# Kernel optimization log

Hardware: AMD Instinct MI355X
Metric: run time of the kernel (lower is better)

Reference implementation:

```python
import jax, jax.numpy as jnp
import numpy as np

N_NODES = 100000
N_EDGES = 1000000
IN_DIM = 64
OUT_DIM = 64
N_REL = 4


def setup_inputs() -> dict:
    key = jax.random.key(0)
    k1, k2, k3, k4, k5, k6 = jax.random.split(key, 6)
    x = jax.random.normal(k1, (N_NODES, IN_DIM), dtype=jnp.float32)
    edge_index = jax.random.randint(k2, (2, N_EDGES), 0, N_NODES, dtype=jnp.int64)
    edge_type = jax.random.randint(k3, (N_EDGES,), 0, N_REL, dtype=jnp.int64)
    # learned params of FastRGCNConv (no basis/block decomposition)
    scale = 1.0 / np.sqrt(IN_DIM)
    weight = jax.random.normal(k4, (N_REL, IN_DIM, OUT_DIM), dtype=jnp.float32) * scale
    root = jax.random.normal(k5, (IN_DIM, OUT_DIM), dtype=jnp.float32) * scale
    bias = jax.random.normal(k6, (OUT_DIM,), dtype=jnp.float32) * 0.01
    return {"x": x, "edge_index": edge_index, "edge_type": edge_type,
            "weight": weight, "root": root, "bias": bias}


def reference(x, edge_index, edge_type, weight, root, bias):
    # FastRGCNConv (aggr='mean', root_weight=True) + Tanh; dropout in eval mode (identity).
    src, dst = edge_index[0], edge_index[1]
    n = x.shape[0]
    # Transform once per relation, then gather per edge: [R, N, out]
    h = jnp.einsum('ni,rio->rno', x, weight)
    msg = h[edge_type, src]                                   # [E, out]
    agg = jax.ops.segment_sum(msg, dst, num_segments=n)       # [N, out]
    cnt = jax.ops.segment_sum(jnp.ones((msg.shape[0],), x.dtype), dst,
                              num_segments=n)                 # in-degree
    agg = agg / jnp.maximum(cnt, 1.0)[:, None]
    out = agg + x @ root + bias
    return jnp.tanh(out)
```

## Files before the change

### kernel.cpp

```cpp
#include <hip/hip_runtime.h>
#include <hip/hip_fp16.h>
#include <math.h>

#define N_NODES 100000
#define N_EDGES 1000000
#define IN_DIM 64
#define OUT_DIM 64
#define CAP 32
#define NB_BKT 512
#define DPB 196
#define QB 2304
#define BINA_BLOCKS 256
#define BINA_CHUNK 3907

typedef __attribute__((ext_vector_type(8)))  short bf16x8;
typedef __attribute__((ext_vector_type(16))) float f32x16;
typedef __attribute__((ext_vector_type(8)))  unsigned short u16x8;
typedef __attribute__((ext_vector_type(4)))  unsigned short u16x4;

__device__ __forceinline__ unsigned short f2bf(float f) {
    unsigned int u = __float_as_uint(f);
    u = (u + 0x7fffu + ((u >> 16) & 1u)) >> 16;
    return (unsigned short)u;
}
__device__ __forceinline__ float bf2f(unsigned short h) {
    return __uint_as_float(((unsigned int)h) << 16);
}
__device__ __forceinline__ __half2 asH2(unsigned int u) {
    union { unsigned int u; __half2 h; } c; c.u = u; return c.h;
}
__device__ __forceinline__ unsigned int asU32(__half2 h) {
    union { unsigned int u; __half2 h; } c; c.h = h; return c.u;
}

__global__ __launch_bounds__(256) void k_prep(
    const float* __restrict__ x,
    const float* __restrict__ weight, const float* __restrict__ root,
    unsigned short* __restrict__ xb, unsigned short* __restrict__ xh,
    unsigned short* __restrict__ wt_hi, unsigned short* __restrict__ wt_lo,
    int* __restrict__ qcnt)
{
    int u = blockIdx.x * 256 + threadIdx.x;
    if (u < NB_BKT) qcnt[u] = 0;
    if (u < 64 * 320) {
        int n = u / 320, k = u - n * 320;
        float v = (k < 256) ? weight[k * 64 + n] : root[(k - 256) * 64 + n];
        unsigned short h = f2bf(v);
        wt_hi[u] = h;
        wt_lo[u] = f2bf(v - bf2f(h));
    }
    if (u >= N_NODES * 16) return;
    float4 v = *(const float4*)(x + (size_t)u * 4);
    u16x4 hb;
    hb[0] = f2bf(v.x); hb[1] = f2bf(v.y); hb[2] = f2bf(v.z); hb[3] = f2bf(v.w);
    *(u16x4*)(xb + (size_t)u * 4) = hb;
    uint2 st;
    st.x = asU32(__floats2half2_rn(v.x, v.y));
    st.y = asU32(__floats2half2_rn(v.z, v.w));
    *(uint2*)(xh + (size_t)u * 4) = st;
}

__global__ __launch_bounds__(512) void k_binA(const int* __restrict__ ei,
                                              const int* __restrict__ et,
                                              int* __restrict__ qcnt,
                                              unsigned int* __restrict__ queue) {
    __shared__ int hist[NB_BKT], base[NB_BKT], cur[NB_BKT];
    int tid = threadIdx.x;
    for (int b = tid; b < NB_BKT; b += 512) { hist[b] = 0; cur[b] = 0; }
    __syncthreads();
    int b0 = blockIdx.x * BINA_CHUNK;
    int b1 = b0 + BINA_CHUNK; if (b1 > N_EDGES) b1 = N_EDGES;
    for (int e = b0 + tid; e < b1; e += 512)
        atomicAdd(&hist[ei[N_EDGES + e] / DPB], 1);
    __syncthreads();
    for (int b = tid; b < NB_BKT; b += 512)
        base[b] = atomicAdd(&qcnt[b], hist[b]);
    __syncthreads();
    for (int e = b0 + tid; e < b1; e += 512) {
        int d = ei[N_EDGES + e];
        int bkt = d / DPB;
        int ld = d - bkt * DPB;
        int pos = base[bkt] + atomicAdd(&cur[bkt], 1);
        if (pos < QB) {
            queue[(size_t)bkt * QB + pos] =
                ((unsigned)ld << 19) | (unsigned)((ei[e] << 2) | (et[e] & 3));
        }
    }
}

__global__ __launch_bounds__(256) void k_binB(const int* __restrict__ qcnt,
                                              const unsigned int* __restrict__ queue,
                                              int* __restrict__ cnt,
                                              int* __restrict__ slots) {
    __shared__ int lcnt[DPB];
    __shared__ int lslot[DPB * CAP];
    int tid = threadIdx.x;
    int bkt = blockIdx.x;
    int d0 = bkt * DPB;
    for (int i = tid; i < DPB; i += 256) lcnt[i] = 0;
    __syncthreads();
    int n = qcnt[bkt]; if (n > QB) n = QB;
    const unsigned int* q = queue + (size_t)bkt * QB;
    for (int i = tid; i < n; i += 256) {
        unsigned int r = q[i];
        int d = (int)(r >> 19);
        int pos = atomicAdd(&lcnt[d], 1);
        if (pos < CAP) lslot[(d << 5) + pos] = (int)(r & 0x7ffffu);
    }
    __syncthreads();
    for (int i = tid; i < DPB; i += 256) {
        int g = d0 + i;
        if (g < N_NODES) cnt[g] = lcnt[i];
    }
    for (int i = tid; i < DPB * CAP / 4; i += 256) {
        int g0 = d0 * CAP + i * 4;
        if (g0 < N_NODES * CAP) {
            int4 v = *(const int4*)&lslot[i * 4];
            *(int4*)&slots[g0] = v;
        }
    }
}

__global__ __launch_bounds__(256) void k_gather(
    const int* __restrict__ cnt, const int* __restrict__ slots,
    const unsigned short* __restrict__ xh, unsigned short* __restrict__ agg)
{
    int wv = threadIdx.x >> 6, ln = threadIdx.x & 63;
    int node = blockIdx.x * 4 + wv;
    int es = ln >> 4;
    int fq = ln & 15;

    int deg = cnt[node];
    int m = (deg < CAP) ? deg : CAP;
    float inv = 1.0f / fmaxf((float)deg, 1.0f);

    int sv = slots[(node << 5) + (ln & 31)];

    __half2 a0_01 = asH2(0), a0_23 = asH2(0);
    __half2 a1_01 = asH2(0), a1_23 = asH2(0);
    __half2 a2_01 = asH2(0), a2_23 = asH2(0);
    __half2 a3_01 = asH2(0), a3_23 = asH2(0);

    int T = (m + 3) >> 2;
    for (int t = 0; t < T; ++t) {
        int i = es + (t << 2);
        int p = __shfl(sv, i);
        bool valid = (i < m);
        if (!valid) p = 0;
        int r = p & 3;
        uint2 v = *(const uint2*)(xh + ((size_t)(p >> 2) << 6) + (fq << 2));
        __half2 h01 = asH2(v.x), h23 = asH2(v.y);
        __half2 m0 = asH2((valid && r == 0) ? 0x3C003C00u : 0u);
        __half2 m1 = asH2((valid && r == 1) ? 0x3C003C00u : 0u);
        __half2 m2 = asH2((valid && r == 2) ? 0x3C003C00u : 0u);
        __half2 m3 = asH2((valid && r == 3) ? 0x3C003C00u : 0u);
        a0_01 = __hfma2(h01, m0, a0_01); a0_23 = __hfma2(h23, m0, a0_23);
        a1_01 = __hfma2(h01, m1, a1_01); a1_23 = __hfma2(h23, m1, a1_23);
        a2_01 = __hfma2(h01, m2, a2_01); a2_23 = __hfma2(h23, m2, a2_23);
        a3_01 = __hfma2(h01, m3, a3_01); a3_23 = __hfma2(h23, m3, a3_23);
    }

#define REDH(a)                                                        \
    a = __hadd2(a, asH2(__shfl_xor(asU32(a), 16)));                    \
    a = __hadd2(a, asH2(__shfl_xor(asU32(a), 32)));
    REDH(a0_01) REDH(a0_23) REDH(a1_01) REDH(a1_23)
    REDH(a2_01) REDH(a2_23) REDH(a3_01) REDH(a3_23)
#undef REDH

    __half2 w01 = a0_01, w23 = a0_23;
    if (es == 1)      { w01 = a1_01; w23 = a1_23; }
    else if (es == 2) { w01 = a2_01; w23 = a2_23; }
    else if (es == 3) { w01 = a3_01; w23 = a3_23; }
    float2 f01 = __half22float2(w01);
    float2 f23 = __half22float2(w23);
    u16x4 h;
    h[0] = f2bf(f01.x * inv); h[1] = f2bf(f01.y * inv);
    h[2] = f2bf(f23.x * inv); h[3] = f2bf(f23.y * inv);
    *(u16x4*)(agg + (size_t)node * 256 + (ln << 2)) = h;
}

__global__ __launch_bounds__(256) void k_gemm(
    const unsigned short* __restrict__ agg,
    const unsigned short* __restrict__ xb,
    const unsigned short* __restrict__ wt_hi,
    const unsigned short* __restrict__ wt_lo,
    const float* __restrict__ bias, float* __restrict__ out)
{
    __shared__ short As[128 * 64];
    __shared__ short Bh[64 * 64];
    __shared__ short Bl[64 * 64];

    int tid = threadIdx.x;
    int n0 = blockIdx.x * 128;
    int lane = tid & 63, wv = tid >> 6;
    int lr = lane & 31, g = lane >> 5;

    f32x16 acc0 = {}, acc1 = {};

    for (int kc = 0; kc < 5; ++kc) {
        if (kc) __syncthreads();
        #pragma unroll
        for (int i = 0; i < 4; ++i) {
            int u = i * 256 + tid;
            int row = u >> 3, i16 = u & 7;
            int node = n0 + row;
            if (node > N_NODES - 1) node = N_NODES - 1;
            const unsigned short* src = (kc < 4)
                ? (agg + (size_t)node * 256 + kc * 64)
                : (xb + (size_t)node * 64);
            u16x8 v = *(const u16x8*)(src + i16 * 8);
            int off = row * 128 + ((i16 * 16) ^ ((row & 7) << 4));
            *(u16x8*)((char*)As + off) = v;
        }
        #pragma unroll
        for (int i = 0; i < 2; ++i) {
            int u = i * 256 + tid;
            int n = u >> 3, i16 = u & 7;
            size_t s = (size_t)n * 320 + kc * 64 + i16 * 8;
            int off = n * 128 + ((i16 * 16) ^ ((n & 7) << 4));
            *(u16x8*)((char*)Bh + off) = *(const u16x8*)(wt_hi + s);
            *(u16x8*)((char*)Bl + off) = *(const u16x8*)(wt_lo + s);
        }
        __syncthreads();
        int ar = wv * 32 + lr;
        #pragma unroll
        for (int kst = 0; kst < 4; ++kst) {
            int kb = kst * 32 + g * 16;
            int offA = ar * 128 + (kb ^ ((ar & 7) << 4));
            int offB = lr * 128 + (kb ^ ((lr & 7) << 4));
            bf16x8 ah  = *(const bf16x8*)((const char*)As + offA);
            bf16x8 bh0 = *(const bf16x8*)((const char*)Bh + offB);
            bf16x8 bl0 = *(const bf16x8*)((const char*)Bl + offB);
            bf16x8 bh1 = *(const bf16x8*)((const char*)Bh + offB + 32 * 128);
            bf16x8 bl1 = *(const bf16x8*)((const char*)Bl + offB + 32 * 128);
            acc0 = __builtin_amdgcn_mfma_f32_32x32x16_bf16(ah, bh0, acc0, 0, 0, 0);
            acc0 = __builtin_amdgcn_mfma_f32_32x32x16_bf16(ah, bl0, acc0, 0, 0, 0);
            acc1 = __builtin_amdgcn_mfma_f32_32x32x16_bf16(ah, bh1, acc1, 0, 0, 0);
            acc1 = __builtin_amdgcn_mfma_f32_32x32x16_bf16(ah, bl1, acc1, 0, 0, 0);
        }
    }

    float b0 = bias[lr], b1 = bias[32 + lr];
    #pragma unroll
    for (int r = 0; r < 16; ++r) {
        int rowl = (r & 3) + ((r >> 2) << 3) + (g << 2);
        int node = n0 + wv * 32 + rowl;
        if (node < N_NODES) {
            out[(size_t)node * 64 + lr]      = tanhf(acc0[r] + b0);
            out[(size_t)node * 64 + 32 + lr] = tanhf(acc1[r] + b1);
        }
    }
}

extern "C" void kernel_launch(void* const* d_in, const int* in_sizes, int n_in,
                              void* d_out, int out_size, void* d_ws, size_t ws_size,
                              hipStream_t stream) {
    const float* x      = (const float*)d_in[0];
    const int*   ei     = (const int*)d_in[1];
    const int*   et     = (const int*)d_in[2];
    const float* weight = (const float*)d_in[3];
    const float* root   = (const float*)d_in[4];
    const float* bias   = (const float*)d_in[5];
    float* out = (float*)d_out;

    unsigned short* agg   = (unsigned short*)d_ws;
    unsigned short* xb    = agg + (size_t)N_NODES * 256;
    unsigned short* xh    = xb + (size_t)N_NODES * 64;
    unsigned short* wt_hi = xh + (size_t)N_NODES * 64;
    unsigned short* wt_lo = wt_hi + 64 * 320;
    int* cnt   = (int*)(wt_lo + 64 * 320);
    int* slots = cnt + N_NODES;
    int* qcnt  = slots + (size_t)N_NODES * CAP;
    unsigned int* queue = (unsigned int*)(qcnt + NB_BKT);

    k_prep<<<(N_NODES * 16 + 255) / 256, 256, 0, stream>>>(x, weight, root,
                                                           xb, xh, wt_hi, wt_lo,
                                                           qcnt);
    k_binA<<<BINA_BLOCKS, 512, 0, stream>>>(ei, et, qcnt, queue);
    k_binB<<<NB_BKT, 256, 0, stream>>>(qcnt, queue, cnt, slots);
    k_gather<<<N_NODES / 4, 256, 0, stream>>>(cnt, slots, xh, agg);
    k_gemm<<<(N_NODES + 127) / 128, 256, 0, stream>>>(agg, xb, wt_hi, wt_lo,
                                                      bias, out);
}
```

Baseline: 97.12 us.

## Sort edge slots by relation in binning and merge prep with edge binning

Fuses the x/weight conversion kernel with the edge-binning kernel into one launch, branching on block index, and zeroes the queue counters with a memset. The second binning pass now counts edges per (node, relation), prefix-sums the counts, and stores each node's slots grouped by relation with packed per-relation offsets in cnt. The gather kernel can then give each 16-lane group a contiguous run of same-relation edges, so it keeps one accumulator pair instead of four masked ones and skips the cross-group shuffle reduction. In exchange binB reads its queue twice, and packing offsets into 8-bit fields caps the stored total degree at 255, which could break the mean for very high-degree nodes.

```diff
diff --git a/kernel.cpp b/kernel.cpp
--- a/kernel.cpp
+++ b/kernel.cpp
@@ -12,6 +12,7 @@
 #define QB 2304
 #define BINA_BLOCKS 256
 #define BINA_CHUNK 3907
+#define PREP_BLOCKS 3125
 
 typedef __attribute__((ext_vector_type(8)))  short bf16x8;
 typedef __attribute__((ext_vector_type(16))) float f32x16;
@@ -33,57 +34,57 @@
     union { unsigned int u; __half2 h; } c; c.h = h; return c.u;
 }
 
-__global__ __launch_bounds__(256) void k_prep(
+__global__ __launch_bounds__(512) void k_prepA(
     const float* __restrict__ x,
     const float* __restrict__ weight, const float* __restrict__ root,
+    const int* __restrict__ ei, const int* __restrict__ et,
     unsigned short* __restrict__ xb, unsigned short* __restrict__ xh,
     unsigned short* __restrict__ wt_hi, unsigned short* __restrict__ wt_lo,
-    int* __restrict__ qcnt)
+    int* __restrict__ qcnt, unsigned int* __restrict__ queue)
 {
-    int u = blockIdx.x * 256 + threadIdx.x;
-    if (u < NB_BKT) qcnt[u] = 0;
-    if (u < 64 * 320) {
-        int n = u / 320, k = u - n * 320;
-        float v = (k < 256) ? weight[k * 64 + n] : root[(k - 256) * 64 + n];
-        unsigned short h = f2bf(v);
-        wt_hi[u] = h;
-        wt_lo[u] = f2bf(v - bf2f(h));
-    }
-    if (u >= N_NODES * 16) return;
-    float4 v = *(const float4*)(x + (size_t)u * 4);
-    u16x4 hb;
-    hb[0] = f2bf(v.x); hb[1] = f2bf(v.y); hb[2] = f2bf(v.z); hb[3] = f2bf(v.w);
-    *(u16x4*)(xb + (size_t)u * 4) = hb;
-    uint2 st;
-    st.x = asU32(__floats2half2_rn(v.x, v.y));
-    st.y = asU32(__floats2half2_rn(v.z, v.w));
-    *(uint2*)(xh + (size_t)u * 4) = st;
-}
-
-__global__ __launch_bounds__(512) void k_binA(const int* __restrict__ ei,
-                                              const int* __restrict__ et,
-                                              int* __restrict__ qcnt,
-                                              unsigned int* __restrict__ queue) {
     __shared__ int hist[NB_BKT], base[NB_BKT], cur[NB_BKT];
     int tid = threadIdx.x;
-    for (int b = tid; b < NB_BKT; b += 512) { hist[b] = 0; cur[b] = 0; }
-    __syncthreads();
-    int b0 = blockIdx.x * BINA_CHUNK;
-    int b1 = b0 + BINA_CHUNK; if (b1 > N_EDGES) b1 = N_EDGES;
-    for (int e = b0 + tid; e < b1; e += 512)
-        atomicAdd(&hist[ei[N_EDGES + e] / DPB], 1);
-    __syncthreads();
-    for (int b = tid; b < NB_BKT; b += 512)
-        base[b] = atomicAdd(&qcnt[b], hist[b]);
-    __syncthreads();
-    for (int e = b0 + tid; e < b1; e += 512) {
-        int d = ei[N_EDGES + e];
-        int bkt = d / DPB;
-        int ld = d - bkt * DPB;
-        int pos = base[bkt] + atomicAdd(&cur[bkt], 1);
-        if (pos < QB) {
-            queue[(size_t)bkt * QB + pos] =
-                ((unsigned)ld << 19) | (unsigned)((ei[e] << 2) | (et[e] & 3));
+
+    if (blockIdx.x < BINA_BLOCKS) {
+        for (int b = tid; b < NB_BKT; b += 512) { hist[b] = 0; cur[b] = 0; }
+        __syncthreads();
+        int b0 = blockIdx.x * BINA_CHUNK;
+        int b1 = b0 + BINA_CHUNK; if (b1 > N_EDGES) b1 = N_EDGES;
+        for (int e = b0 + tid; e < b1; e += 512)
+            atomicAdd(&hist[ei[N_EDGES + e] / DPB], 1);
+        __syncthreads();
+        for (int b = tid; b < NB_BKT; b += 512)
+            base[b] = atomicAdd(&qcnt[b], hist[b]);
+        __syncthreads();
+        for (int e = b0 + tid; e < b1; e += 512) {
+            int d = ei[N_EDGES + e];
+            int bkt = d / DPB;
+            int ld = d - bkt * DPB;
+            int pos = base[bkt] + atomicAdd(&cur[bkt], 1);
+            if (pos < QB) {
+                queue[(size_t)bkt * QB + pos] =
+                    ((unsigned)ld << 19) | (unsigned)((ei[e] << 2) | (et[e] & 3));
+            }
+        }
+    } else {
+        int u = (blockIdx.x - BINA_BLOCKS) * 512 + tid;
+        if (u < 64 * 320) {
+            int n = u / 320, k = u - n * 320;
+            float v = (k < 256) ? weight[k * 64 + n] : root[(k - 256) * 64 + n];
+            unsigned short h = f2bf(v);
+            wt_hi[u] = h;
+            wt_lo[u] = f2bf(v - bf2f(h));
+        }
+        if (u < N_NODES * 16) {
+            float4 v = *(const float4*)(x + (size_t)u * 4);
+            u16x4 hb;
+            hb[0] = f2bf(v.x); hb[1] = f2bf(v.y);
+            hb[2] = f2bf(v.z); hb[3] = f2bf(v.w);
+            *(u16x4*)(xb + (size_t)u * 4) = hb;
+            uint2 st;
+            st.x = asU32(__floats2half2_rn(v.x, v.y));
+            st.y = asU32(__floats2half2_rn(v.z, v.w));
+            *(uint2*)(xh + (size_t)u * 4) = st;
         }
     }
 }
@@ -92,26 +93,43 @@
                                               const unsigned int* __restrict__ queue,
                                               int* __restrict__ cnt,
                                               int* __restrict__ slots) {
-    __shared__ int lcnt[DPB];
+    __shared__ int lc[DPB * 4];
+    __shared__ int lnx[DPB * 4];
     __shared__ int lslot[DPB * CAP];
     int tid = threadIdx.x;
     int bkt = blockIdx.x;
     int d0 = bkt * DPB;
-    for (int i = tid; i < DPB; i += 256) lcnt[i] = 0;
+    for (int i = tid; i < DPB * 4; i += 256) lc[i] = 0;
+    for (int i = tid; i < DPB * CAP; i += 256) lslot[i] = 0;
     __syncthreads();
     int n = qcnt[bkt]; if (n > QB) n = QB;
     const unsigned int* q = queue + (size_t)bkt * QB;
     for (int i = tid; i < n; i += 256) {
         unsigned int r = q[i];
-        int d = (int)(r >> 19);
-        int pos = atomicAdd(&lcnt[d], 1);
-        if (pos < CAP) lslot[(d << 5) + pos] = (int)(r & 0x7ffffu);
-    }
-    __syncthreads();
-    for (int i = tid; i < DPB; i += 256) {
-        int g = d0 + i;
-        if (g < N_NODES) cnt[g] = lcnt[i];
-    }
+        atomicAdd(&lc[(int)(r >> 19) * 4 + (int)(r & 3u)], 1);
+    }
+    __syncthreads();
+    for (int d = tid; d < DPB; d += 256) {
+        int c0 = lc[d * 4], c1 = lc[d * 4 + 1], c2 = lc[d * 4 + 2], c3 = lc[d * 4 + 3];
+        int t1 = c0, t2 = c0 + c1, t3 = t2 + c2, t4 = t3 + c3;
+        int o1 = min(t1, CAP), o2 = min(t2, CAP), o3 = min(t3, CAP), o4 = min(t4, CAP);
+        lnx[d * 4 + 0] = o1; lnx[d * 4 + 1] = o2;
+        lnx[d * 4 + 2] = o3; lnx[d * 4 + 3] = o4;
+        lc[d * 4 + 0] = 0;  lc[d * 4 + 1] = o1;
+        lc[d * 4 + 2] = o2; lc[d * 4 + 3] = o3;
+        int g = d0 + d;
+        if (g < N_NODES)
+            cnt[g] = o1 | (o2 << 8) | (o3 << 16) | (min(t4, 255) << 24);
+    }
+    __syncthreads();
+    for (int i = tid; i < n; i += 256) {
+        unsigned int r = q[i];
+        int d = (int)(r >> 19), rel = (int)(r & 3u);
+        int pos = atomicAdd(&lc[d * 4 + rel], 1);
+        if (pos < lnx[d * 4 + rel])
+            lslot[(d << 5) + pos] = (int)((r >> 2) & 0x1ffffu);
+    }
+    __syncthreads();
     for (int i = tid; i < DPB * CAP / 4; i += 256) {
         int g0 = d0 * CAP + i * 4;
         if (g0 < N_NODES * CAP) {
@@ -130,49 +148,33 @@
     int es = ln >> 4;
     int fq = ln & 15;
 
-    int deg = cnt[node];
-    int m = (deg < CAP) ? deg : CAP;
-    float inv = 1.0f / fmaxf((float)deg, 1.0f);
+    int pk = cnt[node];
+    int o1 = pk & 255, o2 = (pk >> 8) & 255, o3 = (pk >> 16) & 255;
+    int degt = (int)((unsigned)pk >> 24);
+    int o4 = (degt < CAP) ? degt : CAP;
+    float inv = 1.0f / fmaxf((float)degt, 1.0f);
+
+    int s = (es == 0) ? 0 : (es == 1) ? o1 : (es == 2) ? o2 : o3;
+    int e = (es == 0) ? o1 : (es == 1) ? o2 : (es == 2) ? o3 : o4;
+    int c0 = o1, c1 = o2 - o1, c2 = o3 - o2, c3 = o4 - o3;
+    int T = max(max(c0, c1), max(c2, c3));
 
     int sv = slots[(node << 5) + (ln & 31)];
 
-    __half2 a0_01 = asH2(0), a0_23 = asH2(0);
-    __half2 a1_01 = asH2(0), a1_23 = asH2(0);
-    __half2 a2_01 = asH2(0), a2_23 = asH2(0);
-    __half2 a3_01 = asH2(0), a3_23 = asH2(0);
-
-    int T = (m + 3) >> 2;
+    __half2 a01 = asH2(0), a23 = asH2(0);
     for (int t = 0; t < T; ++t) {
-        int i = es + (t << 2);
-        int p = __shfl(sv, i);
-        bool valid = (i < m);
+        int i = s + t;
+        bool valid = (i < e);
+        int p = __shfl(sv, i & 31);
         if (!valid) p = 0;
-        int r = p & 3;
-        uint2 v = *(const uint2*)(xh + ((size_t)(p >> 2) << 6) + (fq << 2));
-        __half2 h01 = asH2(v.x), h23 = asH2(v.y);
-        __half2 m0 = asH2((valid && r == 0) ? 0x3C003C00u : 0u);
-        __half2 m1 = asH2((valid && r == 1) ? 0x3C003C00u : 0u);
-        __half2 m2 = asH2((valid && r == 2) ? 0x3C003C00u : 0u);
-        __half2 m3 = asH2((valid && r == 3) ? 0x3C003C00u : 0u);
-        a0_01 = __hfma2(h01, m0, a0_01); a0_23 = __hfma2(h23, m0, a0_23);
-        a1_01 = __hfma2(h01, m1, a1_01); a1_23 = __hfma2(h23, m1, a1_23);
-        a2_01 = __hfma2(h01, m2, a2_01); a2_23 = __hfma2(h23, m2, a2_23);
-        a3_01 = __hfma2(h01, m3, a3_01); a3_23 = __hfma2(h23, m3, a3_23);
-    }
-
-#define REDH(a)                                                        \
-    a = __hadd2(a, asH2(__shfl_xor(asU32(a), 16)));                    \
-    a = __hadd2(a, asH2(__shfl_xor(asU32(a), 32)));
-    REDH(a0_01) REDH(a0_23) REDH(a1_01) REDH(a1_23)
-    REDH(a2_01) REDH(a2_23) REDH(a3_01) REDH(a3_23)
-#undef REDH
-
-    __half2 w01 = a0_01, w23 = a0_23;
-    if (es == 1)      { w01 = a1_01; w23 = a1_23; }
-    else if (es == 2) { w01 = a2_01; w23 = a2_23; }
-    else if (es == 3) { w01 = a3_01; w23 = a3_23; }
-    float2 f01 = __half22float2(w01);
-    float2 f23 = __half22float2(w23);
+        uint2 v = *(const uint2*)(xh + ((size_t)p << 6) + (fq << 2));
+        __half2 msk = asH2(valid ? 0x3C003C00u : 0u);
+        a01 = __hfma2(asH2(v.x), msk, a01);
+        a23 = __hfma2(asH2(v.y), msk, a23);
+    }
+
+    float2 f01 = __half22float2(a01);
+    float2 f23 = __half22float2(a23);
     u16x4 h;
     h[0] = f2bf(f01.x * inv); h[1] = f2bf(f01.y * inv);
     h[2] = f2bf(f23.x * inv); h[3] = f2bf(f23.y * inv);
@@ -273,10 +275,9 @@
     int* qcnt  = slots + (size_t)N_NODES * CAP;
     unsigned int* queue = (unsigned int*)(qcnt + NB_BKT);
 
-    k_prep<<<(N_NODES * 16 + 255) / 256, 256, 0, stream>>>(x, weight, root,
-                                                           xb, xh, wt_hi, wt_lo,
-                                                           qcnt);
-    k_binA<<<BINA_BLOCKS, 512, 0, stream>>>(ei, et, qcnt, queue);
+    hipMemsetAsync(qcnt, 0, NB_BKT * sizeof(int), stream);
+    k_prepA<<<BINA_BLOCKS + PREP_BLOCKS, 512, 0, stream>>>(
+        x, weight, root, ei, et, xb, xh, wt_hi, wt_lo, qcnt, queue);
     k_binB<<<NB_BKT, 256, 0, stream>>>(qcnt, queue, cnt, slots);
     k_gather<<<N_NODES / 4, 256, 0, stream>>>(cnt, slots, xh, agg);
     k_gemm<<<(N_NODES + 127) / 128, 256, 0, stream>>>(agg, xb, wt_hi, wt_lo,
```

Result: slower. 100.2 us (+3.2%).
